# Performance work log

Hardware: AMD Instinct MI355X
Metric: run time of the kernel (lower is better)

Reference implementation:

```python
import jax, jax.numpy as jnp
import numpy as np

N_NODES = 100000
N_EDGES = 3200000
IN_CH, HID_CH, OUT_CH = 128, 128, 64


def setup_inputs() -> dict:
    key = jax.random.key(0)
    k1, k2, k3, k4 = jax.random.split(key, 4)
    x = jax.random.normal(k1, (N_NODES, IN_CH), dtype=jnp.float32)
    edge_index = jax.random.randint(k2, (2, N_EDGES), 0, N_NODES, dtype=jnp.int64)
    # Glorot-ish scaled weights
    W1 = jax.random.normal(k3, (IN_CH, HID_CH), dtype=jnp.float32) / np.sqrt(IN_CH)
    b1 = jnp.zeros((HID_CH,), dtype=jnp.float32)
    W2 = jax.random.normal(k4, (HID_CH, OUT_CH), dtype=jnp.float32) / np.sqrt(HID_CH)
    b2 = jnp.zeros((OUT_CH,), dtype=jnp.float32)
    return {"x": x, "edge_index": edge_index, "W1": W1, "b1": b1, "W2": W2, "b2": b2}


def _gcn_conv(x, src, dst, norm, W, b, n_nodes):
    # Linear transform first (PyG GCNConv order), then normalized scatter-add aggregation.
    h = x @ W                                   # [N, out]
    msg = norm[:, None] * h[src]                # [E_tot, out] gather + per-edge scale
    out = jax.ops.segment_sum(msg, dst, num_segments=n_nodes)
    return out + b


def reference(x, edge_index, W1, b1, W2, b2):
    n = x.shape[0]
    loop = jnp.arange(n, dtype=edge_index.dtype)
    src = jnp.concatenate([edge_index[0], loop])  # add self-loops (GCNConv default)
    dst = jnp.concatenate([edge_index[1], loop])
    # symmetric normalization: deg computed on dst with unit edge weights
    deg = jax.ops.segment_sum(jnp.ones_like(dst, dtype=x.dtype), dst, num_segments=n)
    dinv = jnp.where(deg > 0, jax.lax.rsqrt(deg), 0.0)
    norm = dinv[src] * dinv[dst]                 # [E_tot]
    h = _gcn_conv(x, src, dst, norm, W1, b1, n)
    h = jax.nn.relu(h)
    z = _gcn_conv(h, src, dst, norm, W2, b2, n)
    return z
```

## Files before the change

kernel.cpp:

```cpp
#include <hip/hip_runtime.h>
#include <cstdint>
#include <cstddef>

static __device__ __forceinline__ unsigned int f2bf_rne(float f) {
    unsigned int u = __float_as_uint(f);
    unsigned int r = 0x7FFFu + ((u >> 16) & 1u);
    return (u + r) >> 16;
}
static __device__ __forceinline__ unsigned int pack_bf2(float lo, float hi) {
    return f2bf_rne(lo) | (f2bf_rne(hi) << 16);
}
static __device__ __forceinline__ float bf_lo(unsigned int w) {
    return __uint_as_float(w << 16);
}
static __device__ __forceinline__ float bf_hi(unsigned int w) {
    return __uint_as_float(w & 0xFFFF0000u);
}

#define BKT_CH 8192


__global__ void k_detect64(const unsigned int* ei, int e, int* is64) {
    __shared__ int nonzero;
    if (threadIdx.x == 0) nonzero = 0;
    __syncthreads();
    for (int i = threadIdx.x; i < 4096; i += blockDim.x) {
        size_t k = (size_t)((unsigned long long)i * (unsigned long long)e / 4096ull);
        if (ei[2 * k + 1] != 0u) nonzero = 1;
    }
    __syncthreads();
    if (threadIdx.x == 0) *is64 = nonzero ? 0 : 1;
}

__global__ void k_zero512(int* p) { p[threadIdx.x] = 0; }

__global__ __launch_bounds__(256) void k_hist(const void* ei_raw, int e, const int* is64,
                                              int* __restrict__ bkt_cnt) {
    __shared__ int lcnt[512];
    int t = threadIdx.x;
    for (int j = t; j < 512; j += 256) lcnt[j] = 0;
    __syncthreads();
    int lo = blockIdx.x * BKT_CH;
    int hi = lo + BKT_CH; if (hi > e) hi = e;
    if (*is64) {
        const long long* p = (const long long*)ei_raw;
        for (int i = lo + t; i < hi; i += 256)
            atomicAdd(&lcnt[((int)p[(size_t)e + i]) >> 8], 1);
    } else {
        const int* p = (const int*)ei_raw;
        for (int i = lo + t; i < hi; i += 256)
            atomicAdd(&lcnt[p[(size_t)e + i] >> 8], 1);
    }
    __syncthreads();
    for (int j = t; j < 512; j += 256)
        if (lcnt[j]) atomicAdd(&bkt_cnt[j], lcnt[j]);
}

__global__ __launch_bounds__(512) void k_scan_bkt(const int* __restrict__ bkt_cnt,
                                                  int* __restrict__ bkt_base,
                                                  int* __restrict__ bkt_cursor, int nb) {
    __shared__ int s[512];
    int t = threadIdx.x;
    int v = (t < nb) ? bkt_cnt[t] : 0;
    s[t] = v;
    __syncthreads();
    #pragma unroll
    for (int d = 1; d < 512; d <<= 1) {
        int tmp = (t >= d) ? s[t - d] : 0;
        __syncthreads();
        s[t] += tmp;
        __syncthreads();
    }
    if (t < nb) {
        int b = s[t] - v;
        bkt_base[t]   = b;
        bkt_cursor[t] = b;
    }
    if (t == 511) bkt_base[nb] = s[511];
}

__global__ __launch_bounds__(256) void k_bucket(const void* ei_raw, int e, const int* is64,
                                                int* __restrict__ bkt_cursor,
                                                unsigned int* __restrict__ pout) {
    __shared__ int ldst[BKT_CH];
    __shared__ int lsrc[BKT_CH];
    __shared__ int lcnt[512];
    __shared__ int lbase[512];
    int t = threadIdx.x;
    int lo = blockIdx.x * BKT_CH;
    int hi = lo + BKT_CH; if (hi > e) hi = e;
    int m = hi - lo;
    for (int j = t; j < 512; j += 256) lcnt[j] = 0;
    __syncthreads();
    bool w64 = (*is64 != 0);
    const long long* p64 = (const long long*)ei_raw;
    const int*       p32 = (const int*)ei_raw;
    for (int idx = t; idx < m; idx += 256) {
        size_t i = (size_t)lo + idx;
        int s, d;
        if (w64) { s = (int)p64[i]; d = (int)p64[(size_t)e + i]; }
        else     { s = p32[i];      d = p32[(size_t)e + i]; }
        ldst[idx] = d;
        lsrc[idx] = s;
        atomicAdd(&lcnt[d >> 8], 1);
    }
    __syncthreads();
    for (int j = t; j < 512; j += 256) {
        int c = lcnt[j];
        lbase[j] = c ? atomicAdd(&bkt_cursor[j], c) : 0;
        lcnt[j] = 0;
    }
    __syncthreads();
    for (int idx = t; idx < m; idx += 256) {
        int d = ldst[idx], s = lsrc[idx];
        int b = d >> 8;
        int pos = lbase[b] + atomicAdd(&lcnt[b], 1);
        pout[pos] = ((unsigned int)(d & 255) << 24) | (unsigned int)s;
    }
}

__global__ __launch_bounds__(256) void k_place_deg(const unsigned int* __restrict__ pairs,
                                                   const int* __restrict__ bkt_base,
                                                   int n, int nb,
                                                   int* __restrict__ row_ptr,
                                                   float* __restrict__ dinv,
                                                   int* __restrict__ src_sorted) {
    __shared__ int lcnt[256];
    __shared__ int ls[256];
    __shared__ int lcur[256];
    int b = blockIdx.x;
    int t = threadIdx.x;
    int base = bkt_base[b], end = bkt_base[b + 1];
    lcnt[t] = 0;
    __syncthreads();
    for (int i = base + t; i < end; i += 256)
        atomicAdd(&lcnt[__builtin_nontemporal_load(&pairs[i]) >> 24], 1);
    __syncthreads();
    int v = lcnt[t];
    ls[t] = v;
    __syncthreads();
    #pragma unroll
    for (int d = 1; d < 256; d <<= 1) {
        int tmp = (t >= d) ? ls[t - d] : 0;
        __syncthreads();
        ls[t] += tmp;
        __syncthreads();
    }
    int nodebase = base + ls[t] - v;
    int node = (b << 8) + t;
    if (node < n) {
        row_ptr[node] = nodebase;
        dinv[node] = rsqrtf((float)(v + 1));
    }
    lcur[t] = nodebase;
    __syncthreads();
    for (int i = base + t; i < end; i += 256) {
        unsigned int pr = __builtin_nontemporal_load(&pairs[i]);
        int pos = atomicAdd(&lcur[pr >> 24], 1);
        src_sorted[pos] = (int)(pr & 0x00FFFFFFu);
    }
    if (t == 0 && b == nb - 1) row_ptr[n] = end;
}


__global__ __launch_bounds__(256) void k_gemm128(const float* __restrict__ A,
                                                 const float* __restrict__ W,
                                                 const float* __restrict__ dinv,
                                                 unsigned int* __restrict__ hsb, int M) {
    __shared__ float sA[64][36];
    __shared__ float sW[32][128];
    int tid = threadIdx.x;
    int tx = tid & 15;
    int ty = tid >> 4;
    int row0 = blockIdx.x * 64;
    float acc[4][8] = {};
    for (int k0 = 0; k0 < 128; k0 += 32) {
        __syncthreads();
        for (int i = tid; i < 512; i += 256) {
            int r = i >> 3, c4 = i & 7;
            float4 v = {0.f, 0.f, 0.f, 0.f};
            int gr = row0 + r;
            if (gr < M) v = *reinterpret_cast<const float4*>(&A[(size_t)gr * 128 + k0 + c4 * 4]);
            *reinterpret_cast<float4*>(&sA[r][c4 * 4]) = v;
        }
        for (int i = tid; i < 1024; i += 256) {
            int r = i >> 5, c4 = i & 31;
            *reinterpret_cast<float4*>(&sW[r][c4 * 4]) =
                *reinterpret_cast<const float4*>(&W[(size_t)(k0 + r) * 128 + c4 * 4]);
        }
        __syncthreads();
        #pragma unroll
        for (int k = 0; k < 32; k += 4) {
            float4 a[4];
            #pragma unroll
            for (int r = 0; r < 4; ++r)
                a[r] = *reinterpret_cast<const float4*>(&sA[ty * 4 + r][k]);
            #pragma unroll
            for (int kk = 0; kk < 4; ++kk) {
                float4 w0 = *reinterpret_cast<const float4*>(&sW[k + kk][tx * 8]);
                float4 w1 = *reinterpret_cast<const float4*>(&sW[k + kk][tx * 8 + 4]);
                #pragma unroll
                for (int r = 0; r < 4; ++r) {
                    float av = (&a[r].x)[kk];
                    acc[r][0] += av * w0.x; acc[r][1] += av * w0.y;
                    acc[r][2] += av * w0.z; acc[r][3] += av * w0.w;
                    acc[r][4] += av * w1.x; acc[r][5] += av * w1.y;
                    acc[r][6] += av * w1.z; acc[r][7] += av * w1.w;
                }
            }
        }
    }
    #pragma unroll
    for (int r = 0; r < 4; ++r) {
        int gr = row0 + ty * 4 + r;
        if (gr < M) {
            float di = dinv[gr];
            uint4 o;
            o.x = pack_bf2(acc[r][0] * di, acc[r][1] * di);
            o.y = pack_bf2(acc[r][2] * di, acc[r][3] * di);
            o.z = pack_bf2(acc[r][4] * di, acc[r][5] * di);
            o.w = pack_bf2(acc[r][6] * di, acc[r][7] * di);
            *reinterpret_cast<uint4*>(&hsb[(size_t)gr * 64 + tx * 4]) = o;
        }
    }
}

__global__ __launch_bounds__(256) void k_gemm64(const unsigned int* __restrict__ Ab,
                                                const float* __restrict__ W,
                                                const float* __restrict__ dinv,
                                                unsigned int* __restrict__ zsb, int M) {
    __shared__ float sA[64][36];
    __shared__ float sW[32][64];
    int tid = threadIdx.x;
    int tx = tid & 15;
    int ty = tid >> 4;
    int row0 = blockIdx.x * 64;
    float acc[4][4] = {};
    for (int k0 = 0; k0 < 128; k0 += 32) {
        __syncthreads();
        for (int i = tid; i < 1024; i += 256) {
            int r = i >> 4, w = i & 15;
            int gr = row0 + r;
            unsigned int pv = (gr < M) ? Ab[(size_t)gr * 64 + (k0 >> 1) + w] : 0u;
            sA[r][2 * w]     = bf_lo(pv);
            sA[r][2 * w + 1] = bf_hi(pv);
        }
        for (int i = tid; i < 512; i += 256) {
            int r = i >> 4, c4 = i & 15;
            *reinterpret_cast<float4*>(&sW[r][c4 * 4]) =
                *reinterpret_cast<const float4*>(&W[(size_t)(k0 + r) * 64 + c4 * 4]);
        }
        __syncthreads();
        #pragma unroll
        for (int k = 0; k < 32; k += 4) {
            float4 a[4];
            #pragma unroll
            for (int r = 0; r < 4; ++r)
                a[r] = *reinterpret_cast<const float4*>(&sA[ty * 4 + r][k]);
            #pragma unroll
            for (int kk = 0; kk < 4; ++kk) {
                float4 w = *reinterpret_cast<const float4*>(&sW[k + kk][tx * 4]);
                #pragma unroll
                for (int r = 0; r < 4; ++r) {
                    float av = (&a[r].x)[kk];
                    acc[r][0] += av * w.x; acc[r][1] += av * w.y;
                    acc[r][2] += av * w.z; acc[r][3] += av * w.w;
                }
            }
        }
    }
    #pragma unroll
    for (int r = 0; r < 4; ++r) {
        int gr = row0 + ty * 4 + r;
        if (gr < M) {
            float di = dinv[gr];
            uint2 o;
            o.x = pack_bf2(acc[r][0] * di, acc[r][1] * di);
            o.y = pack_bf2(acc[r][2] * di, acc[r][3] * di);
            *reinterpret_cast<uint2*>(&zsb[(size_t)gr * 32 + tx * 2]) = o;
        }
    }
}


__global__ __launch_bounds__(64) void k_agg1(const unsigned int* __restrict__ hsb,
                                             const float* __restrict__ dinv,
                                             const int* __restrict__ row_ptr,
                                             const int* __restrict__ src_sorted,
                                             const float* __restrict__ b1,
                                             unsigned int* __restrict__ h2b) {
    int i = blockIdx.x;
    int c = threadIdx.x;
    unsigned int w = hsb[(size_t)i * 64 + c];
    float ax = bf_lo(w), ay = bf_hi(w);
    int lo = row_ptr[i], hi = row_ptr[i + 1];
    int e = lo;
    for (; e + 8 <= hi; e += 8) {
        int s0 = __builtin_nontemporal_load(&src_sorted[e + 0]);
        int s1 = __builtin_nontemporal_load(&src_sorted[e + 1]);
        int s2 = __builtin_nontemporal_load(&src_sorted[e + 2]);
        int s3 = __builtin_nontemporal_load(&src_sorted[e + 3]);
        int s4 = __builtin_nontemporal_load(&src_sorted[e + 4]);
        int s5 = __builtin_nontemporal_load(&src_sorted[e + 5]);
        int s6 = __builtin_nontemporal_load(&src_sorted[e + 6]);
        int s7 = __builtin_nontemporal_load(&src_sorted[e + 7]);
        unsigned int w0 = hsb[(size_t)s0 * 64 + c];
        unsigned int w1 = hsb[(size_t)s1 * 64 + c];
        unsigned int w2 = hsb[(size_t)s2 * 64 + c];
        unsigned int w3 = hsb[(size_t)s3 * 64 + c];
        unsigned int w4 = hsb[(size_t)s4 * 64 + c];
        unsigned int w5 = hsb[(size_t)s5 * 64 + c];
        unsigned int w6 = hsb[(size_t)s6 * 64 + c];
        unsigned int w7 = hsb[(size_t)s7 * 64 + c];
        ax += ((bf_lo(w0) + bf_lo(w1)) + (bf_lo(w2) + bf_lo(w3)))
            + ((bf_lo(w4) + bf_lo(w5)) + (bf_lo(w6) + bf_lo(w7)));
        ay += ((bf_hi(w0) + bf_hi(w1)) + (bf_hi(w2) + bf_hi(w3)))
            + ((bf_hi(w4) + bf_hi(w5)) + (bf_hi(w6) + bf_hi(w7)));
    }
    if (e + 4 <= hi) {
        int s0 = __builtin_nontemporal_load(&src_sorted[e + 0]);
        int s1 = __builtin_nontemporal_load(&src_sorted[e + 1]);
        int s2 = __builtin_nontemporal_load(&src_sorted[e + 2]);
        int s3 = __builtin_nontemporal_load(&src_sorted[e + 3]);
        unsigned int w0 = hsb[(size_t)s0 * 64 + c];
        unsigned int w1 = hsb[(size_t)s1 * 64 + c];
        unsigned int w2 = hsb[(size_t)s2 * 64 + c];
        unsigned int w3 = hsb[(size_t)s3 * 64 + c];
        ax += (bf_lo(w0) + bf_lo(w1)) + (bf_lo(w2) + bf_lo(w3));
        ay += (bf_hi(w0) + bf_hi(w1)) + (bf_hi(w2) + bf_hi(w3));
        e += 4;
    }
    for (; e < hi; ++e) {
        int s = __builtin_nontemporal_load(&src_sorted[e]);
        unsigned int ws = hsb[(size_t)s * 64 + c];
        ax += bf_lo(ws);
        ay += bf_hi(ws);
    }
    float di = dinv[i];
    float2 bb = *reinterpret_cast<const float2*>(&b1[2 * c]);
    float v0 = di * ax + bb.x;
    float v1 = di * ay + bb.y;
    unsigned int pv = pack_bf2(v0 > 0.f ? v0 : 0.f, v1 > 0.f ? v1 : 0.f);
    __builtin_nontemporal_store(pv, &h2b[(size_t)i * 64 + c]);
}

__global__ __launch_bounds__(64) void k_agg2(const unsigned int* __restrict__ zsb,
                                             const float* __restrict__ dinv,
                                             const int* __restrict__ row_ptr,
                                             const int* __restrict__ src_sorted,
                                             const float* __restrict__ b2,
                                             float* __restrict__ out, int n) {
    int i = blockIdx.x * 2 + (threadIdx.x >> 5);
    int c = threadIdx.x & 31;
    if (i >= n) return;
    unsigned int w = zsb[(size_t)i * 32 + c];
    float ax = bf_lo(w), ay = bf_hi(w);
    int lo = row_ptr[i], hi = row_ptr[i + 1];
    int e = lo;
    for (; e + 8 <= hi; e += 8) {
        int s0 = __builtin_nontemporal_load(&src_sorted[e + 0]);
        int s1 = __builtin_nontemporal_load(&src_sorted[e + 1]);
        int s2 = __builtin_nontemporal_load(&src_sorted[e + 2]);
        int s3 = __builtin_nontemporal_load(&src_sorted[e + 3]);
        int s4 = __builtin_nontemporal_load(&src_sorted[e + 4]);
        int s5 = __builtin_nontemporal_load(&src_sorted[e + 5]);
        int s6 = __builtin_nontemporal_load(&src_sorted[e + 6]);
        int s7 = __builtin_nontemporal_load(&src_sorted[e + 7]);
        unsigned int w0 = zsb[(size_t)s0 * 32 + c];
        unsigned int w1 = zsb[(size_t)s1 * 32 + c];
        unsigned int w2 = zsb[(size_t)s2 * 32 + c];
        unsigned int w3 = zsb[(size_t)s3 * 32 + c];
        unsigned int w4 = zsb[(size_t)s4 * 32 + c];
        unsigned int w5 = zsb[(size_t)s5 * 32 + c];
        unsigned int w6 = zsb[(size_t)s6 * 32 + c];
        unsigned int w7 = zsb[(size_t)s7 * 32 + c];
        ax += ((bf_lo(w0) + bf_lo(w1)) + (bf_lo(w2) + bf_lo(w3)))
            + ((bf_lo(w4) + bf_lo(w5)) + (bf_lo(w6) + bf_lo(w7)));
        ay += ((bf_hi(w0) + bf_hi(w1)) + (bf_hi(w2) + bf_hi(w3)))
            + ((bf_hi(w4) + bf_hi(w5)) + (bf_hi(w6) + bf_hi(w7)));
    }
    if (e + 4 <= hi) {
        int s0 = __builtin_nontemporal_load(&src_sorted[e + 0]);
        int s1 = __builtin_nontemporal_load(&src_sorted[e + 1]);
        int s2 = __builtin_nontemporal_load(&src_sorted[e + 2]);
        int s3 = __builtin_nontemporal_load(&src_sorted[e + 3]);
        unsigned int w0 = zsb[(size_t)s0 * 32 + c];
        unsigned int w1 = zsb[(size_t)s1 * 32 + c];
        unsigned int w2 = zsb[(size_t)s2 * 32 + c];
        unsigned int w3 = zsb[(size_t)s3 * 32 + c];
        ax += (bf_lo(w0) + bf_lo(w1)) + (bf_lo(w2) + bf_lo(w3));
        ay += (bf_hi(w0) + bf_hi(w1)) + (bf_hi(w2) + bf_hi(w3));
        e += 4;
    }
    for (; e < hi; ++e) {
        int s = __builtin_nontemporal_load(&src_sorted[e]);
        unsigned int ws = zsb[(size_t)s * 32 + c];
        ax += bf_lo(ws);
        ay += bf_hi(ws);
    }
    float di = dinv[i];
    float2 bb = *reinterpret_cast<const float2*>(&b2[2 * c]);
    float2 o = {di * ax + bb.x, di * ay + bb.y};
    *reinterpret_cast<float2*>(&out[(size_t)i * 64 + 2 * c]) = o;
}


static inline size_t alignup(size_t v) { return (v + 255) & ~(size_t)255; }

extern "C" void kernel_launch(void* const* d_in, const int* in_sizes, int n_in,
                              void* d_out, int out_size, void* d_ws, size_t ws_size,
                              hipStream_t stream) {
    const float* x  = (const float*)d_in[0];
    const void*  ei = d_in[1];
    const float* W1 = (const float*)d_in[2];
    const float* b1 = (const float*)d_in[3];
    const float* W2 = (const float*)d_in[4];
    const float* b2 = (const float*)d_in[5];

    const int n = in_sizes[0] / 128;
    const int e = in_sizes[1] / 2;

    char* p = (char*)d_ws;
    auto take = [&](size_t bytes) { char* q = p; p += alignup(bytes); return q; };
    size_t pairs_bytes = (size_t)e * 4;
    size_t hsb_bytes   = (size_t)n * 64 * 4;
    size_t regA_bytes  = pairs_bytes > hsb_bytes ? pairs_bytes : hsb_bytes;
    char* regA = (char*)take(regA_bytes);
    unsigned int* pairs = (unsigned int*)regA;
    unsigned int* hsb   = (unsigned int*)regA;

    unsigned int* h2b        = (unsigned int*)take((size_t)n * 64 * 4);
    int*          is64       = (int*)  take(4);
    float*        dinv       = (float*)take((size_t)n * 4);
    int*          row_ptr    = (int*)  take((size_t)(n + 1) * 4);
    int*          bkt_cnt    = (int*)  take(512 * 4);
    int*          bkt_base   = (int*)  take(513 * 4);
    int*          bkt_cursor = (int*)  take(512 * 4);
    int*          src_sorted = (int*)  take((size_t)e * 4);
    unsigned int* zsb        = (unsigned int*)take((size_t)n * 32 * 4);
    if ((size_t)(p - (char*)d_ws) > ws_size) return;

    const int nb_bkt  = (n + 255) >> 8;
    const int nb_chnk = (e + BKT_CH - 1) / BKT_CH;

    k_detect64<<<1, 256, 0, stream>>>((const unsigned int*)ei, e, is64);
    k_zero512<<<1, 512, 0, stream>>>(bkt_cnt);
    k_hist<<<nb_chnk, 256, 0, stream>>>(ei, e, is64, bkt_cnt);
    k_scan_bkt<<<1, 512, 0, stream>>>(bkt_cnt, bkt_base, bkt_cursor, nb_bkt);
    k_bucket<<<nb_chnk, 256, 0, stream>>>(ei, e, is64, bkt_cursor, pairs);
    k_place_deg<<<nb_bkt, 256, 0, stream>>>(pairs, bkt_base, n, nb_bkt,
                                            row_ptr, dinv, src_sorted);

    k_gemm128<<<(n + 63) / 64, 256, 0, stream>>>(x, W1, dinv, hsb, n);
    k_agg1<<<n, 64, 0, stream>>>(hsb, dinv, row_ptr, src_sorted, b1, h2b);
    k_gemm64<<<(n + 63) / 64, 256, 0, stream>>>(h2b, W2, dinv, zsb, n);
    k_agg2<<<(n + 1) / 2, 64, 0, stream>>>(zsb, dinv, row_ptr, src_sorted, b2, (float*)d_out, n);
}
```

Before: 353.9 us.

## Fuse layer-1 aggregation with layer-2 GEMM through shared memory

Replaces the separate k_agg1 and k_gemm64 kernels with one kernel. Each 256-thread block first aggregates 64 nodes, with each wave handling 16 nodes sequentially, and keeps the ReLU'd hidden rows in fp32 shared memory. It then runs the 128x64 GEMM directly from that shared tile. This removes the h2b round trip through global memory and one launch. In exchange, each wave walks 16 nodes serially, which lowers the number of gathers in flight per block. The larger shared tile may also reduce occupancy for this gather-bound phase.

```diff
diff --git a/kernel.cpp b/kernel.cpp
--- a/kernel.cpp
+++ b/kernel.cpp
@@ -161,7 +161,6 @@
     }
     if (t == 0 && b == nb - 1) row_ptr[n] = end;
 }
-
 
 __global__ __launch_bounds__(256) void k_gemm128(const float* __restrict__ A,
                                                  const float* __restrict__ W,
@@ -225,30 +224,91 @@
     }
 }
 
-__global__ __launch_bounds__(256) void k_gemm64(const unsigned int* __restrict__ Ab,
-                                                const float* __restrict__ W,
+__global__ __launch_bounds__(256) void k_fused1(const unsigned int* __restrict__ hsb,
                                                 const float* __restrict__ dinv,
-                                                unsigned int* __restrict__ zsb, int M) {
-    __shared__ float sA[64][36];
+                                                const int* __restrict__ row_ptr,
+                                                const int* __restrict__ src_sorted,
+                                                const float* __restrict__ b1,
+                                                const float* __restrict__ W2,
+                                                unsigned int* __restrict__ zsb, int n) {
+    __shared__ float h2s[64][132];
     __shared__ float sW[32][64];
     int tid = threadIdx.x;
+    int w   = tid >> 6;
+    int c   = tid & 63;
+    int row0 = blockIdx.x * 64;
+
+    float2 bb = *reinterpret_cast<const float2*>(&b1[2 * c]);
+    for (int j = 0; j < 16; ++j) {
+        int il = w * 16 + j;
+        int i  = row0 + il;
+        float v0 = 0.f, v1 = 0.f;
+        if (i < n) {
+            unsigned int wd = hsb[(size_t)i * 64 + c];
+            float ax = bf_lo(wd), ay = bf_hi(wd);
+            int lo = row_ptr[i], hi = row_ptr[i + 1];
+            int e = lo;
+            for (; e + 8 <= hi; e += 8) {
+                int s0 = __builtin_nontemporal_load(&src_sorted[e + 0]);
+                int s1 = __builtin_nontemporal_load(&src_sorted[e + 1]);
+                int s2 = __builtin_nontemporal_load(&src_sorted[e + 2]);
+                int s3 = __builtin_nontemporal_load(&src_sorted[e + 3]);
+                int s4 = __builtin_nontemporal_load(&src_sorted[e + 4]);
+                int s5 = __builtin_nontemporal_load(&src_sorted[e + 5]);
+                int s6 = __builtin_nontemporal_load(&src_sorted[e + 6]);
+                int s7 = __builtin_nontemporal_load(&src_sorted[e + 7]);
+                unsigned int w0 = hsb[(size_t)s0 * 64 + c];
+                unsigned int w1 = hsb[(size_t)s1 * 64 + c];
+                unsigned int w2 = hsb[(size_t)s2 * 64 + c];
+                unsigned int w3 = hsb[(size_t)s3 * 64 + c];
+                unsigned int w4 = hsb[(size_t)s4 * 64 + c];
+                unsigned int w5 = hsb[(size_t)s5 * 64 + c];
+                unsigned int w6 = hsb[(size_t)s6 * 64 + c];
+                unsigned int w7 = hsb[(size_t)s7 * 64 + c];
+                ax += ((bf_lo(w0) + bf_lo(w1)) + (bf_lo(w2) + bf_lo(w3)))
+                    + ((bf_lo(w4) + bf_lo(w5)) + (bf_lo(w6) + bf_lo(w7)));
+                ay += ((bf_hi(w0) + bf_hi(w1)) + (bf_hi(w2) + bf_hi(w3)))
+                    + ((bf_hi(w4) + bf_hi(w5)) + (bf_hi(w6) + bf_hi(w7)));
+            }
+            if (e + 4 <= hi) {
+                int s0 = __builtin_nontemporal_load(&src_sorted[e + 0]);
+                int s1 = __builtin_nontemporal_load(&src_sorted[e + 1]);
+                int s2 = __builtin_nontemporal_load(&src_sorted[e + 2]);
+                int s3 = __builtin_nontemporal_load(&src_sorted[e + 3]);
+                unsigned int w0 = hsb[(size_t)s0 * 64 + c];
+                unsigned int w1 = hsb[(size_t)s1 * 64 + c];
+                unsigned int w2 = hsb[(size_t)s2 * 64 + c];
+                unsigned int w3 = hsb[(size_t)s3 * 64 + c];
+                ax += (bf_lo(w0) + bf_lo(w1)) + (bf_lo(w2) + bf_lo(w3));
+                ay += (bf_hi(w0) + bf_hi(w1)) + (bf_hi(w2) + bf_hi(w3));
+                e += 4;
+            }
+            for (; e < hi; ++e) {
+                int s = __builtin_nontemporal_load(&src_sorted[e]);
+                unsigned int ws = hsb[(size_t)s * 64 + c];
+                ax += bf_lo(ws);
+                ay += bf_hi(ws);
+            }
+            float di = dinv[i];
+            v0 = di * ax + bb.x;
+            v1 = di * ay + bb.y;
+            v0 = v0 > 0.f ? v0 : 0.f;
+            v1 = v1 > 0.f ? v1 : 0.f;
+        }
+        float2 o = {v0, v1};
+        *reinterpret_cast<float2*>(&h2s[il][2 * c]) = o;
+    }
+    __syncthreads();
+
     int tx = tid & 15;
     int ty = tid >> 4;
-    int row0 = blockIdx.x * 64;
     float acc[4][4] = {};
     for (int k0 = 0; k0 < 128; k0 += 32) {
         __syncthreads();
-        for (int i = tid; i < 1024; i += 256) {
-            int r = i >> 4, w = i & 15;
-            int gr = row0 + r;
-            unsigned int pv = (gr < M) ? Ab[(size_t)gr * 64 + (k0 >> 1) + w] : 0u;
-            sA[r][2 * w]     = bf_lo(pv);
-            sA[r][2 * w + 1] = bf_hi(pv);
-        }
         for (int i = tid; i < 512; i += 256) {
             int r = i >> 4, c4 = i & 15;
             *reinterpret_cast<float4*>(&sW[r][c4 * 4]) =
-                *reinterpret_cast<const float4*>(&W[(size_t)(k0 + r) * 64 + c4 * 4]);
+                *reinterpret_cast<const float4*>(&W2[(size_t)(k0 + r) * 64 + c4 * 4]);
         }
         __syncthreads();
         #pragma unroll
@@ -256,15 +316,15 @@
             float4 a[4];
             #pragma unroll
             for (int r = 0; r < 4; ++r)
-                a[r] = *reinterpret_cast<const float4*>(&sA[ty * 4 + r][k]);
+                a[r] = *reinterpret_cast<const float4*>(&h2s[ty * 4 + r][k0 + k]);
             #pragma unroll
             for (int kk = 0; kk < 4; ++kk) {
-                float4 w = *reinterpret_cast<const float4*>(&sW[k + kk][tx * 4]);
+                float4 wv = *reinterpret_cast<const float4*>(&sW[k + kk][tx * 4]);
                 #pragma unroll
                 for (int r = 0; r < 4; ++r) {
                     float av = (&a[r].x)[kk];
-                    acc[r][0] += av * w.x; acc[r][1] += av * w.y;
-                    acc[r][2] += av * w.z; acc[r][3] += av * w.w;
+                    acc[r][0] += av * wv.x; acc[r][1] += av * wv.y;
+                    acc[r][2] += av * wv.z; acc[r][3] += av * wv.w;
                 }
             }
         }
@@ -272,7 +332,7 @@
     #pragma unroll
     for (int r = 0; r < 4; ++r) {
         int gr = row0 + ty * 4 + r;
-        if (gr < M) {
+        if (gr < n) {
             float di = dinv[gr];
             uint2 o;
             o.x = pack_bf2(acc[r][0] * di, acc[r][1] * di);
@@ -280,68 +340,6 @@
             *reinterpret_cast<uint2*>(&zsb[(size_t)gr * 32 + tx * 2]) = o;
         }
     }
-}
-
-
-__global__ __launch_bounds__(64) void k_agg1(const unsigned int* __restrict__ hsb,
-                                             const float* __restrict__ dinv,
-                                             const int* __restrict__ row_ptr,
-                                             const int* __restrict__ src_sorted,
-                                             const float* __restrict__ b1,
-                                             unsigned int* __restrict__ h2b) {
-    int i = blockIdx.x;
-    int c = threadIdx.x;
-    unsigned int w = hsb[(size_t)i * 64 + c];
-    float ax = bf_lo(w), ay = bf_hi(w);
-    int lo = row_ptr[i], hi = row_ptr[i + 1];
-    int e = lo;
-    for (; e + 8 <= hi; e += 8) {
-        int s0 = __builtin_nontemporal_load(&src_sorted[e + 0]);
-        int s1 = __builtin_nontemporal_load(&src_sorted[e + 1]);
-        int s2 = __builtin_nontemporal_load(&src_sorted[e + 2]);
-        int s3 = __builtin_nontemporal_load(&src_sorted[e + 3]);
-        int s4 = __builtin_nontemporal_load(&src_sorted[e + 4]);
-        int s5 = __builtin_nontemporal_load(&src_sorted[e + 5]);
-        int s6 = __builtin_nontemporal_load(&src_sorted[e + 6]);
-        int s7 = __builtin_nontemporal_load(&src_sorted[e + 7]);
-        unsigned int w0 = hsb[(size_t)s0 * 64 + c];
-        unsigned int w1 = hsb[(size_t)s1 * 64 + c];
-        unsigned int w2 = hsb[(size_t)s2 * 64 + c];
-        unsigned int w3 = hsb[(size_t)s3 * 64 + c];
-        unsigned int w4 = hsb[(size_t)s4 * 64 + c];
-        unsigned int w5 = hsb[(size_t)s5 * 64 + c];
-        unsigned int w6 = hsb[(size_t)s6 * 64 + c];
-        unsigned int w7 = hsb[(size_t)s7 * 64 + c];
-        ax += ((bf_lo(w0) + bf_lo(w1)) + (bf_lo(w2) + bf_lo(w3)))
-            + ((bf_lo(w4) + bf_lo(w5)) + (bf_lo(w6) + bf_lo(w7)));
-        ay += ((bf_hi(w0) + bf_hi(w1)) + (bf_hi(w2) + bf_hi(w3)))
-            + ((bf_hi(w4) + bf_hi(w5)) + (bf_hi(w6) + bf_hi(w7)));
-    }
-    if (e + 4 <= hi) {
-        int s0 = __builtin_nontemporal_load(&src_sorted[e + 0]);
-        int s1 = __builtin_nontemporal_load(&src_sorted[e + 1]);
-        int s2 = __builtin_nontemporal_load(&src_sorted[e + 2]);
-        int s3 = __builtin_nontemporal_load(&src_sorted[e + 3]);
-        unsigned int w0 = hsb[(size_t)s0 * 64 + c];
-        unsigned int w1 = hsb[(size_t)s1 * 64 + c];
-        unsigned int w2 = hsb[(size_t)s2 * 64 + c];
-        unsigned int w3 = hsb[(size_t)s3 * 64 + c];
-        ax += (bf_lo(w0) + bf_lo(w1)) + (bf_lo(w2) + bf_lo(w3));
-        ay += (bf_hi(w0) + bf_hi(w1)) + (bf_hi(w2) + bf_hi(w3));
-        e += 4;
-    }
-    for (; e < hi; ++e) {
-        int s = __builtin_nontemporal_load(&src_sorted[e]);
-        unsigned int ws = hsb[(size_t)s * 64 + c];
-        ax += bf_lo(ws);
-        ay += bf_hi(ws);
-    }
-    float di = dinv[i];
-    float2 bb = *reinterpret_cast<const float2*>(&b1[2 * c]);
-    float v0 = di * ax + bb.x;
-    float v1 = di * ay + bb.y;
-    unsigned int pv = pack_bf2(v0 > 0.f ? v0 : 0.f, v1 > 0.f ? v1 : 0.f);
-    __builtin_nontemporal_store(pv, &h2b[(size_t)i * 64 + c]);
 }
 
 __global__ __launch_bounds__(64) void k_agg2(const unsigned int* __restrict__ zsb,
@@ -429,7 +427,6 @@
     unsigned int* pairs = (unsigned int*)regA;
     unsigned int* hsb   = (unsigned int*)regA;
 
-    unsigned int* h2b        = (unsigned int*)take((size_t)n * 64 * 4);
     int*          is64       = (int*)  take(4);
     float*        dinv       = (float*)take((size_t)n * 4);
     int*          row_ptr    = (int*)  take((size_t)(n + 1) * 4);
@@ -452,7 +449,7 @@
                                             row_ptr, dinv, src_sorted);
 
     k_gemm128<<<(n + 63) / 64, 256, 0, stream>>>(x, W1, dinv, hsb, n);
-    k_agg1<<<n, 64, 0, stream>>>(hsb, dinv, row_ptr, src_sorted, b1, h2b);
-    k_gemm64<<<(n + 63) / 64, 256, 0, stream>>>(h2b, W2, dinv, zsb, n);
+    k_fused1<<<(n + 63) / 64, 256, 0, stream>>>(hsb, dinv, row_ptr, src_sorted,
+                                                b1, W2, zsb, n);
     k_agg2<<<(n + 1) / 2, 64, 0, stream>>>(zsb, dinv, row_ptr, src_sorted, b2, (float*)d_out, n);
 }
```

Result: slower. 487.9 us (+37.9%).

## Use bf16 MFMA instructions for both dense transform GEMMs

Applied to the files above, without the earlier changes.

Both node-feature GEMMs now convert the A tile and weights to bf16 in shared memory and compute with 16x16x32 bf16 MFMA instructions instead of scalar FP32 FMAs. The whole K=128 tile is staged once, with no K loop. The epilogue uses lane shuffles to pair columns before writing packed bf16. The intent is to cut GEMM compute time, at the cost of lower-precision inputs to the first layer and scattered 4-byte output stores.

```diff
diff --git a/kernel.cpp b/kernel.cpp
--- a/kernel.cpp
+++ b/kernel.cpp
@@ -1,6 +1,9 @@
 #include <hip/hip_runtime.h>
 #include <cstdint>
 #include <cstddef>
+
+typedef short bf16x8 __attribute__((ext_vector_type(8)));
+typedef float f32x4  __attribute__((ext_vector_type(4)));
 
 static __device__ __forceinline__ unsigned int f2bf_rne(float f) {
     unsigned int u = __float_as_uint(f);
@@ -162,65 +165,63 @@
     if (t == 0 && b == nb - 1) row_ptr[n] = end;
 }
 
-
 __global__ __launch_bounds__(256) void k_gemm128(const float* __restrict__ A,
                                                  const float* __restrict__ W,
                                                  const float* __restrict__ dinv,
                                                  unsigned int* __restrict__ hsb, int M) {
-    __shared__ float sA[64][36];
-    __shared__ float sW[32][128];
+    __shared__ unsigned int A_lds[64][68];
+    __shared__ unsigned int B_lds[16 * 128 * 4];
     int tid = threadIdx.x;
-    int tx = tid & 15;
-    int ty = tid >> 4;
+    int w   = tid >> 6;
+    int l   = tid & 63;
     int row0 = blockIdx.x * 64;
-    float acc[4][8] = {};
-    for (int k0 = 0; k0 < 128; k0 += 32) {
-        __syncthreads();
-        for (int i = tid; i < 512; i += 256) {
-            int r = i >> 3, c4 = i & 7;
-            float4 v = {0.f, 0.f, 0.f, 0.f};
-            int gr = row0 + r;
-            if (gr < M) v = *reinterpret_cast<const float4*>(&A[(size_t)gr * 128 + k0 + c4 * 4]);
-            *reinterpret_cast<float4*>(&sA[r][c4 * 4]) = v;
+
+    for (int idx = tid; idx < 4096; idx += 256) {
+        int r = idx >> 6, kp = idx & 63;
+        unsigned int pv = 0u;
+        int gr = row0 + r;
+        if (gr < M) {
+            float2 f = *reinterpret_cast<const float2*>(&A[(size_t)gr * 128 + 2 * kp]);
+            pv = pack_bf2(f.x, f.y);
         }
-        for (int i = tid; i < 1024; i += 256) {
-            int r = i >> 5, c4 = i & 31;
-            *reinterpret_cast<float4*>(&sW[r][c4 * 4]) =
-                *reinterpret_cast<const float4*>(&W[(size_t)(k0 + r) * 128 + c4 * 4]);
+        A_lds[r][kp] = pv;
+    }
+    for (int idx = tid; idx < 8192; idx += 256) {
+        int col = idx & 127, kp = idx >> 7;
+        float v0 = W[(size_t)(2 * kp) * 128 + col];
+        float v1 = W[(size_t)(2 * kp + 1) * 128 + col];
+        B_lds[(((kp >> 2) * 128) + col) * 4 + (kp & 3)] = pack_bf2(v0, v1);
+    }
+    __syncthreads();
+
+    int arow = w * 16 + (l & 15);
+    int kq   = (l >> 4);
+    f32x4 acc[8];
+    #pragma unroll
+    for (int nb = 0; nb < 8; ++nb) acc[nb] = (f32x4){0.f, 0.f, 0.f, 0.f};
+
+    #pragma unroll
+    for (int k0 = 0; k0 < 4; ++k0) {
+        bf16x8 af = *reinterpret_cast<const bf16x8*>(&A_lds[arow][k0 * 16 + kq * 4]);
+        #pragma unroll
+        for (int nb = 0; nb < 8; ++nb) {
+            const unsigned int* bp = &B_lds[(((k0 * 4 + kq) * 128) + nb * 16 + (l & 15)) * 4];
+            bf16x8 bf = *reinterpret_cast<const bf16x8*>(bp);
+            acc[nb] = __builtin_amdgcn_mfma_f32_16x16x32_bf16(af, bf, acc[nb], 0, 0, 0);
         }
-        __syncthreads();
+    }
+
+    #pragma unroll
+    for (int r = 0; r < 4; ++r) {
+        int gr = row0 + w * 16 + (l >> 4) * 4 + r;
+        float di = (gr < M) ? dinv[gr] : 0.f;
         #pragma unroll
-        for (int k = 0; k < 32; k += 4) {
-            float4 a[4];
-            #pragma unroll
-            for (int r = 0; r < 4; ++r)
-                a[r] = *reinterpret_cast<const float4*>(&sA[ty * 4 + r][k]);
-            #pragma unroll
-            for (int kk = 0; kk < 4; ++kk) {
-                float4 w0 = *reinterpret_cast<const float4*>(&sW[k + kk][tx * 8]);
-                float4 w1 = *reinterpret_cast<const float4*>(&sW[k + kk][tx * 8 + 4]);
-                #pragma unroll
-                for (int r = 0; r < 4; ++r) {
-                    float av = (&a[r].x)[kk];
-                    acc[r][0] += av * w0.x; acc[r][1] += av * w0.y;
-                    acc[r][2] += av * w0.z; acc[r][3] += av * w0.w;
-                    acc[r][4] += av * w1.x; acc[r][5] += av * w1.y;
-                    acc[r][6] += av * w1.z; acc[r][7] += av * w1.w;
-                }
+        for (int nb = 0; nb < 8; ++nb) {
+            float fv = acc[nb][r] * di;
+            float pv = __shfl_xor(fv, 1);
+            if ((l & 1) == 0 && gr < M) {
+                hsb[(size_t)gr * 64 + nb * 8 + ((l & 15) >> 1)] = pack_bf2(fv, pv);
             }
-        }
-    }
-    #pragma unroll
-    for (int r = 0; r < 4; ++r) {
-        int gr = row0 + ty * 4 + r;
-        if (gr < M) {
-            float di = dinv[gr];
-            uint4 o;
-            o.x = pack_bf2(acc[r][0] * di, acc[r][1] * di);
-            o.y = pack_bf2(acc[r][2] * di, acc[r][3] * di);
-            o.z = pack_bf2(acc[r][4] * di, acc[r][5] * di);
-            o.w = pack_bf2(acc[r][6] * di, acc[r][7] * di);
-            *reinterpret_cast<uint4*>(&hsb[(size_t)gr * 64 + tx * 4]) = o;
         }
     }
 }
@@ -229,55 +230,54 @@
                                                 const float* __restrict__ W,
                                                 const float* __restrict__ dinv,
                                                 unsigned int* __restrict__ zsb, int M) {
-    __shared__ float sA[64][36];
-    __shared__ float sW[32][64];
+    __shared__ unsigned int A_lds[64][68];
+    __shared__ unsigned int B_lds[16 * 64 * 4];
     int tid = threadIdx.x;
-    int tx = tid & 15;
-    int ty = tid >> 4;
+    int w   = tid >> 6;
+    int l   = tid & 63;
     int row0 = blockIdx.x * 64;
-    float acc[4][4] = {};
-    for (int k0 = 0; k0 < 128; k0 += 32) {
-        __syncthreads();
-        for (int i = tid; i < 1024; i += 256) {
-            int r = i >> 4, w = i & 15;
-            int gr = row0 + r;
-            unsigned int pv = (gr < M) ? Ab[(size_t)gr * 64 + (k0 >> 1) + w] : 0u;
-            sA[r][2 * w]     = bf_lo(pv);
-            sA[r][2 * w + 1] = bf_hi(pv);
+
+    for (int idx = tid; idx < 4096; idx += 256) {
+        int r = idx >> 6, kp = idx & 63;
+        int gr = row0 + r;
+        A_lds[r][kp] = (gr < M) ? Ab[(size_t)gr * 64 + kp] : 0u;
+    }
+    for (int idx = tid; idx < 4096; idx += 256) {
+        int col = idx & 63, kp = idx >> 6;
+        float v0 = W[(size_t)(2 * kp) * 64 + col];
+        float v1 = W[(size_t)(2 * kp + 1) * 64 + col];
+        B_lds[(((kp >> 2) * 64) + col) * 4 + (kp & 3)] = pack_bf2(v0, v1);
+    }
+    __syncthreads();
+
+    int arow = w * 16 + (l & 15);
+    int kq   = (l >> 4);
+    f32x4 acc[4];
+    #pragma unroll
+    for (int nb = 0; nb < 4; ++nb) acc[nb] = (f32x4){0.f, 0.f, 0.f, 0.f};
+
+    #pragma unroll
+    for (int k0 = 0; k0 < 4; ++k0) {
+        bf16x8 af = *reinterpret_cast<const bf16x8*>(&A_lds[arow][k0 * 16 + kq * 4]);
+        #pragma unroll
+        for (int nb = 0; nb < 4; ++nb) {
+            const unsigned int* bp = &B_lds[(((k0 * 4 + kq) * 64) + nb * 16 + (l & 15)) * 4];
+            bf16x8 bf = *reinterpret_cast<const bf16x8*>(bp);
+            acc[nb] = __builtin_amdgcn_mfma_f32_16x16x32_bf16(af, bf, acc[nb], 0, 0, 0);
         }
-        for (int i = tid; i < 512; i += 256) {
-            int r = i >> 4, c4 = i & 15;
-            *reinterpret_cast<float4*>(&sW[r][c4 * 4]) =
-                *reinterpret_cast<const float4*>(&W[(size_t)(k0 + r) * 64 + c4 * 4]);
-        }
-        __syncthreads();
+    }
+
+    #pragma unroll
+    for (int r = 0; r < 4; ++r) {
+        int gr = row0 + w * 16 + (l >> 4) * 4 + r;
+        float di = (gr < M) ? dinv[gr] : 0.f;
         #pragma unroll
-        for (int k = 0; k < 32; k += 4) {
-            float4 a[4];
-            #pragma unroll
-            for (int r = 0; r < 4; ++r)
-                a[r] = *reinterpret_cast<const float4*>(&sA[ty * 4 + r][k]);
-            #pragma unroll
-            for (int kk = 0; kk < 4; ++kk) {
-                float4 w = *reinterpret_cast<const float4*>(&sW[k + kk][tx * 4]);
-                #pragma unroll
-                for (int r = 0; r < 4; ++r) {
-                    float av = (&a[r].x)[kk];
-                    acc[r][0] += av * w.x; acc[r][1] += av * w.y;
-                    acc[r][2] += av * w.z; acc[r][3] += av * w.w;
-                }
+        for (int nb = 0; nb < 4; ++nb) {
+            float fv = acc[nb][r] * di;
+            float pv = __shfl_xor(fv, 1);
+            if ((l & 1) == 0 && gr < M) {
+                zsb[(size_t)gr * 32 + nb * 8 + ((l & 15) >> 1)] = pack_bf2(fv, pv);
             }
-        }
-    }
-    #pragma unroll
-    for (int r = 0; r < 4; ++r) {
-        int gr = row0 + ty * 4 + r;
-        if (gr < M) {
-            float di = dinv[gr];
-            uint2 o;
-            o.x = pack_bf2(acc[r][0] * di, acc[r][1] * di);
-            o.y = pack_bf2(acc[r][2] * di, acc[r][3] * di);
-            *reinterpret_cast<uint2*>(&zsb[(size_t)gr * 32 + tx * 2]) = o;
         }
     }
 }
```

Measured after the change: 320.4 us. 9.5% less time.
